# Performance work log

Hardware: AMD Instinct MI355X
Metric: run time of the kernel (lower is better)

Reference implementation:

```python
import jax, jax.numpy as jnp
import numpy as np

B, C, H, W = 8, 256, 96, 96
GH, GW = 16, 16                # proto_grid
KH, KW = H // GH, W // GW      # avg-pool kernel = stride
P = GH * GW                    # local prototypes per sample
THRESH = 0.95
NORM_EPS = 1e-4


def _safe_norm(x, axis):
    # L2-normalize with norm clamped below at NORM_EPS (matches safe_norm)
    n = jnp.sqrt(jnp.sum(x * x, axis=axis, keepdims=True))
    return x / jnp.maximum(n, NORM_EPS)


def _avg_pool(x):
    # [B, c, H, W] -> [B, c, P] non-overlapping KHxKW average pooling
    b, c = x.shape[:2]
    return x.reshape(b, c, GH, KH, GW, KW).mean(axis=(3, 5)).reshape(b, c, P)


def setup_inputs() -> dict:
    key = jax.random.key(0)
    k1, k2, k3, k4 = jax.random.split(key, 4)
    qry_fts = jax.random.normal(k1, (B, C, H, W), dtype=jnp.float32)
    sup_fts = jax.random.normal(k2, (B, C, H, W), dtype=jnp.float32)
    sup_mask = (jax.random.uniform(k3, (B, 1, H, W)) > 0.02).astype(jnp.float32)
    true_bg_mask = (jax.random.uniform(k4, (B, 1, H, W)) > 0.9).astype(jnp.float32)
    return {"qry_fts": qry_fts, "sup_fts": sup_fts,
            "sup_mask": sup_mask, "true_bg_mask": true_bg_mask}


def reference(qry_fts, sup_fts, sup_mask, true_bg_mask):
    # mode='gridconv+' path, vectorized: ragged prototype selection -> masked softmax
    local_fts = _avg_pool(sup_fts).transpose(0, 2, 1)       # [B, P, C]
    local_mask = _avg_pool(sup_mask)[:, 0, :]               # [B, P]
    local_bg = _avg_pool(true_bg_mask)[:, 0, :]             # [B, P]
    valid = (local_mask > THRESH) & (local_bg < 0.5)        # [B, P] bool

    # global masked-average prototype
    gproto = jnp.sum(sup_fts * sup_mask, axis=(-1, -2)) / (
        jnp.sum(sup_mask, axis=(-1, -2)) + 1e-5)            # [B, C]

    protos = jnp.concatenate([local_fts, gproto[:, None, :]], axis=1)  # [B, P+1, C]
    valid_all = jnp.concatenate(
        [valid, jnp.ones((B, 1), dtype=bool)], axis=1)      # global always valid

    protos_n = _safe_norm(protos, axis=2)                   # [B, P+1, C]
    qry_n = _safe_norm(qry_fts, axis=1)                     # [B, C, H, W]

    # 1x1 conv with prototype weights == batched cosine similarity
    dists = jnp.einsum('bchw,bpc->bphw', qry_n, protos_n)   # [B, P+1, H, W]

    # softmax restricted to valid prototypes (invalid get weight 0)
    logits = jnp.where(valid_all[:, :, None, None], dists, -jnp.inf)
    w = jax.nn.softmax(logits, axis=1)
    pred = jnp.sum(w * dists, axis=1, keepdims=True)        # [B, 1, H, W]
    return pred
```

## Files before the change

### kernel.cpp

```cpp
#include <hip/hip_runtime.h>

#define BB 8
#define CC 256
#define HH 96
#define WW 96
#define HWW (HH*WW)
#define NLOC 256
#define PPAD 257
#define THRESH 0.95f
#define NORM_EPS 1e-4f

typedef __attribute__((ext_vector_type(8))) _Float16 f16x8;
typedef __attribute__((ext_vector_type(16))) float f32x16;

union H16 { _Float16 f; unsigned short u; };

__global__ void k01(const float* __restrict__ sup_fts,
                    const float* __restrict__ sup_mask,
                    const float* __restrict__ true_bg,
                    float* __restrict__ protos,
                    float* __restrict__ validf,
                    float* __restrict__ masksum) {
    __shared__ float red[256];
    int blk = blockIdx.x;
    int t = threadIdx.x;
    if (blk < BB * CC) {
        int b = blk >> 8, c = blk & 255;
        int gy = t >> 4, gx = t & 15;
        const float* fb = sup_fts + ((size_t)b * CC + c) * HWW;
        const float* mb = sup_mask + (size_t)b * HWW;
        int base = gy * 6 * WW + gx * 6;
        float fs = 0.f, fm = 0.f;
        for (int r = 0; r < 6; ++r) {
            const float* rowf = fb + base + r * WW;
            const float* rowm = mb + base + r * WW;
#pragma unroll
            for (int h = 0; h < 3; ++h) {
                float2 v  = *(const float2*)(rowf + 2 * h);
                float2 mk = *(const float2*)(rowm + 2 * h);
                fs += v.x + v.y;
                fm = fmaf(v.x, mk.x, fm);
                fm = fmaf(v.y, mk.y, fm);
            }
        }
        protos[((size_t)b * PPAD + t) * CC + c] = fs * (1.f / 36.f);
        red[t] = fm;
        __syncthreads();
        for (int off = 128; off > 0; off >>= 1) {
            if (t < off) red[t] += red[t + off];
            __syncthreads();
        }
        if (t == 0) protos[((size_t)b * PPAD + 256) * CC + c] = red[0];
    } else {
        int b = blk - BB * CC;
        int gy = t >> 4, gx = t & 15;
        const float* mb = sup_mask + (size_t)b * HWW;
        const float* gb = true_bg  + (size_t)b * HWW;
        int base = gy * 6 * WW + gx * 6;
        float ms = 0.f, bs = 0.f;
        for (int r = 0; r < 6; ++r) {
            const float* rowm = mb + base + r * WW;
            const float* rowg = gb + base + r * WW;
#pragma unroll
            for (int h = 0; h < 3; ++h) {
                float2 mk = *(const float2*)(rowm + 2 * h);
                float2 bg2 = *(const float2*)(rowg + 2 * h);
                ms += mk.x + mk.y;
                bs += bg2.x + bg2.y;
            }
        }
        float mmean = ms * (1.f / 36.f);
        float bmean = bs * (1.f / 36.f);
        validf[b * PPAD + t] = (mmean > THRESH && bmean < 0.5f) ? 1.f : 0.f;
        if (t == 0) validf[b * PPAD + 256] = 1.f;
        red[t] = ms;
        __syncthreads();
        for (int off = 128; off > 0; off >>= 1) {
            if (t < off) red[t] += red[t + off];
            __syncthreads();
        }
        if (t == 0) masksum[b] = red[0];
    }
}

__global__ void k2_norm(float* __restrict__ protos,
                        const float* __restrict__ masksum,
                        unsigned short* __restrict__ Pimg) {
    int bp = blockIdx.x;
    int b = bp / PPAD;
    int p = bp - b * PPAD;
    int t = threadIdx.x;
    float v = protos[((size_t)b * PPAD + p) * CC + t];
    if (p == 256) v = v / (masksum[b] + 1e-5f);
    __shared__ float red[256];
    red[t] = v * v;
    __syncthreads();
    for (int off = 128; off > 0; off >>= 1) {
        if (t < off) red[t] += red[t + off];
        __syncthreads();
    }
    float norm = sqrtf(red[0]);
    float vn = v / fmaxf(norm, NORM_EPS);
    protos[((size_t)b * PPAD + p) * CC + t] = vn;
    if (p < NLOC) {
        H16 h; h.f = (_Float16)vn;
        int kstep = t >> 4, khalf = (t >> 3) & 1, e = t & 7;
        int tile = p >> 5, col = p & 31;
        size_t idx = ((((size_t)b * 16 + kstep) * 2 + khalf) * 8 + tile) * 256
                     + col * 8 + e;
        Pimg[idx] = h.u;
    }
}

__global__ __launch_bounds__(256, 6)
void k3_mfma(const float* __restrict__ qry,
             const unsigned short* __restrict__ Pimg,
             const float* __restrict__ protos_n,
             const float* __restrict__ validf,
             float* __restrict__ out) {
    __shared__ alignas(16) unsigned short Qf[64 * 128];
    __shared__ float red_n[8][32], red_g[8][32];
    __shared__ float rn_s[32], gd_s[32];
    __shared__ float S_l[4][32], N_l[4][32];

    int blk = blockIdx.x;
    int b = blk & 7;
    int tpx = blk >> 3;
    int px0 = tpx * 32;
    int t = threadIdx.x;
    int l = t & 63;
    int w = t >> 6;
    int col = l & 31;
    int h = l >> 5;

    int spx = t & 31;
    int cg  = t >> 5;

    const float* qb = qry + (size_t)b * CC * HWW + px0 + spx;
    const float* gp = protos_n + ((size_t)b * PPAD + 256) * CC;
    const unsigned short* Pb = Pimg + (size_t)b * 65536;

    float nrm = 0.f, gac = 0.f;
#pragma unroll
    for (int j = 0; j < 8; ++j) {
        int c0 = cg * 32 + j * 4;
        float v[4], gpv[4];
#pragma unroll
        for (int i = 0; i < 4; ++i) { v[i] = qb[(size_t)(c0 + i) * HWW]; gpv[i] = gp[c0 + i]; }
        unsigned int hh[4];
#pragma unroll
        for (int i = 0; i < 4; ++i) {
            H16 x; x.f = (_Float16)v[i];
            hh[i] = x.u;
            nrm = fmaf(v[i], v[i], nrm);
            gac = fmaf(v[i], gpv[i], gac);
        }
        int kq = cg * 8 + j;
        uint2 pk;
        pk.x = hh[0] | (hh[1] << 16); pk.y = hh[2] | (hh[3] << 16);
        *(uint2*)&Qf[kq * 128 + spx * 4] = pk;
    }
    red_n[cg][spx] = nrm;
    red_g[cg][spx] = gac;
    __syncthreads();
    if (t < 32) {
        float n2 = 0.f, gs = 0.f;
#pragma unroll
        for (int i = 0; i < 8; ++i) { n2 += red_n[i][t]; gs += red_g[i][t]; }
        float rn = 1.f / fmaxf(sqrtf(n2), NORM_EPS);
        rn_s[t] = rn;
        gd_s[t] = gs * rn;
    }

    f32x16 acc[2];
#pragma unroll
    for (int i = 0; i < 16; ++i) { acc[0][i] = 0.f; acc[1][i] = 0.f; }
    f16x8 Bf[2][2];

#define LOADB(KS, BUF)                                                        \
    {                                                                         \
        _Pragma("unroll")                                                     \
        for (int ti = 0; ti < 2; ++ti)                                        \
            Bf[BUF][ti] = *(const f16x8*)(Pb +                                \
                ((((size_t)(KS) * 2 + h) * 8 + (w * 2 + ti)) * 32 + col) * 8);\
    }

    LOADB(0, 0);
    LOADB(1, 1);

#pragma unroll
    for (int ks = 0; ks < 16; ++ks) {
        int kq0 = ks * 4 + h * 2;
        uint2 a0 = *(const uint2*)&Qf[kq0 * 128 + col * 4];
        uint2 a1 = *(const uint2*)&Qf[(kq0 + 1) * 128 + col * 4];
        union { f16x8 v; unsigned int u[4]; } QA;
        QA.u[0] = a0.x; QA.u[1] = a0.y; QA.u[2] = a1.x; QA.u[3] = a1.y;
#pragma unroll
        for (int ti = 0; ti < 2; ++ti)
            acc[ti] = __builtin_amdgcn_mfma_f32_32x32x16_f16(QA.v, Bf[ks & 1][ti], acc[ti], 0, 0, 0);
        if (ks + 2 < 16) LOADB(ks + 2, ks & 1);
    }
#undef LOADB

    __syncthreads();

    float vf0 = validf[b * PPAD + w * 64 + col];
    float vf1 = validf[b * PPAD + w * 64 + 32 + col];
#pragma unroll
    for (int r = 0; r < 16; ++r) {
        int row = (r & 3) + 8 * (r >> 2) + 4 * h;
        float rnv = rn_s[row];
        float d0 = acc[0][r] * rnv;
        float d1 = acc[1][r] * rnv;
        float l0 = (vf0 != 0.f) ? d0 : -1e30f;
        float l1 = (vf1 != 0.f) ? d1 : -1e30f;
        float e0 = __expf(l0 - 1.1f);
        float e1 = __expf(l1 - 1.1f);
        float s = e0 + e1;
        float nn = fmaf(e0, l0, e1 * l1);
#pragma unroll
        for (int m = 1; m < 32; m <<= 1) {
            s  += __shfl_xor(s, m);
            nn += __shfl_xor(nn, m);
        }
        if (col == 0) { S_l[w][row] = s; N_l[w][row] = nn; }
    }
    __syncthreads();

    if (t < 32) {
        float gdv = gd_s[t];
        float eg = __expf(gdv - 1.1f);
        float S = eg, N = eg * gdv;
#pragma unroll
        for (int i = 0; i < 4; ++i) { S += S_l[i][t]; N += N_l[i][t]; }
        out[(size_t)b * HWW + px0 + t] = N / S;
    }
}

extern "C" void kernel_launch(void* const* d_in, const int* in_sizes, int n_in,
                              void* d_out, int out_size, void* d_ws, size_t ws_size,
                              hipStream_t stream) {
    const float* qry = (const float*)d_in[0];
    const float* sup = (const float*)d_in[1];
    const float* msk = (const float*)d_in[2];
    const float* bg  = (const float*)d_in[3];
    float* out = (float*)d_out;

    float* ws = (float*)d_ws;
    float* protos  = ws;
    float* validf  = protos + (size_t)BB * PPAD * CC;
    float* masksum = validf + (size_t)BB * PPAD;
    unsigned short* Pimg = (unsigned short*)(masksum + BB);

    hipLaunchKernelGGL(k01, dim3(BB * CC + BB), dim3(256), 0, stream,
                       sup, msk, bg, protos, validf, masksum);
    hipLaunchKernelGGL(k2_norm, dim3(BB * PPAD), dim3(256), 0, stream, protos, masksum, Pimg);
    hipLaunchKernelGGL(k3_mfma, dim3(BB * (HWW / 32)), dim3(256), 0, stream,
                       qry, Pimg, protos, validf, out);
}
```

Baseline: 58.22 us.

## Software-pipeline query loads across three pixel tiles per block with double-buffered LDS

```diff
diff --git a/kernel.cpp b/kernel.cpp
--- a/kernel.cpp
+++ b/kernel.cpp
@@ -112,128 +112,167 @@
     }
 }
 
-__global__ __launch_bounds__(256, 6)
+#define LBAR()  do {                                             \
+        asm volatile("s_waitcnt lgkmcnt(0)" ::: "memory");       \
+        __builtin_amdgcn_sched_barrier(0);                       \
+        __builtin_amdgcn_s_barrier();                            \
+        __builtin_amdgcn_sched_barrier(0);                       \
+    } while (0)
+
+__global__ __launch_bounds__(256, 4)
 void k3_mfma(const float* __restrict__ qry,
              const unsigned short* __restrict__ Pimg,
              const float* __restrict__ protos_n,
              const float* __restrict__ validf,
              float* __restrict__ out) {
-    __shared__ alignas(16) unsigned short Qf[64 * 128];
-    __shared__ float red_n[8][32], red_g[8][32];
-    __shared__ float rn_s[32], gd_s[32];
+    __shared__ alignas(16) unsigned short Qf[2][8192];
+    __shared__ float red_n[2][8][32], red_g[2][8][32];
+    __shared__ float rn_s[2][32], gd_s[2][32];
     __shared__ float S_l[4][32], N_l[4][32];
 
     int blk = blockIdx.x;
     int b = blk & 7;
-    int tpx = blk >> 3;
-    int px0 = tpx * 32;
+    int tgrp = blk >> 3;
+    int pxbase = tgrp * 96;
     int t = threadIdx.x;
     int l = t & 63;
     int w = t >> 6;
     int col = l & 31;
     int h = l >> 5;
-
     int spx = t & 31;
     int cg  = t >> 5;
 
-    const float* qb = qry + (size_t)b * CC * HWW + px0 + spx;
+    const float* qB = qry + (size_t)b * CC * HWW + spx;
     const float* gp = protos_n + ((size_t)b * PPAD + 256) * CC;
     const unsigned short* Pb = Pimg + (size_t)b * 65536;
-
-    float nrm = 0.f, gac = 0.f;
-#pragma unroll
-    for (int j = 0; j < 8; ++j) {
-        int c0 = cg * 32 + j * 4;
-        float v[4], gpv[4];
-#pragma unroll
-        for (int i = 0; i < 4; ++i) { v[i] = qb[(size_t)(c0 + i) * HWW]; gpv[i] = gp[c0 + i]; }
-        unsigned int hh[4];
-#pragma unroll
-        for (int i = 0; i < 4; ++i) {
-            H16 x; x.f = (_Float16)v[i];
-            hh[i] = x.u;
-            nrm = fmaf(v[i], v[i], nrm);
-            gac = fmaf(v[i], gpv[i], gac);
-        }
-        int kq = cg * 8 + j;
-        uint2 pk;
-        pk.x = hh[0] | (hh[1] << 16); pk.y = hh[2] | (hh[3] << 16);
-        *(uint2*)&Qf[kq * 128 + spx * 4] = pk;
-    }
-    red_n[cg][spx] = nrm;
-    red_g[cg][spx] = gac;
-    __syncthreads();
-    if (t < 32) {
-        float n2 = 0.f, gs = 0.f;
-#pragma unroll
-        for (int i = 0; i < 8; ++i) { n2 += red_n[i][t]; gs += red_g[i][t]; }
-        float rn = 1.f / fmaxf(sqrtf(n2), NORM_EPS);
-        rn_s[t] = rn;
-        gd_s[t] = gs * rn;
-    }
-
-    f32x16 acc[2];
-#pragma unroll
-    for (int i = 0; i < 16; ++i) { acc[0][i] = 0.f; acc[1][i] = 0.f; }
-    f16x8 Bf[2][2];
-
-#define LOADB(KS, BUF)                                                        \
-    {                                                                         \
+    float* outb = out + (size_t)b * HWW + pxbase;
+
+    float vfl0 = validf[b * PPAD + w * 64 + col];
+    float vfl1 = validf[b * PPAD + w * 64 + 32 + col];
+
+    {
+        float nrm = 0.f, gac = 0.f;
+        const float* qb = qB + pxbase;
+#pragma unroll
+        for (int j = 0; j < 8; ++j) {
+            int c0 = cg * 32 + j * 4;
+            float v[4];
+#pragma unroll
+            for (int i = 0; i < 4; ++i) v[i] = qb[(size_t)(c0 + i) * HWW];
+            unsigned int hh[4];
+#pragma unroll
+            for (int i = 0; i < 4; ++i) {
+                H16 x; x.f = (_Float16)v[i];
+                hh[i] = x.u;
+                nrm = fmaf(v[i], v[i], nrm);
+                gac = fmaf(v[i], gp[c0 + i], gac);
+            }
+            uint2 pk;
+            pk.x = hh[0] | (hh[1] << 16); pk.y = hh[2] | (hh[3] << 16);
+            *(uint2*)&Qf[0][(cg * 8 + j) * 128 + spx * 4] = pk;
+        }
+        red_n[0][cg][spx] = nrm;
+        red_g[0][cg][spx] = gac;
+    }
+
+#pragma unroll
+    for (int ti = 0; ti < 3; ++ti) {
+        const int p = ti & 1;
+        LBAR();
+        if (t < 32) {
+            float n2 = 0.f, gs = 0.f;
+#pragma unroll
+            for (int i = 0; i < 8; ++i) { n2 += red_n[p][i][t]; gs += red_g[p][i][t]; }
+            float rn = 1.f / fmaxf(sqrtf(n2), NORM_EPS);
+            rn_s[p][t] = rn;
+            gd_s[p][t] = gs * rn;
+        }
+        LBAR();
+
+        f32x16 acc[2];
+#pragma unroll
+        for (int i = 0; i < 16; ++i) { acc[0][i] = 0.f; acc[1][i] = 0.f; }
+        f16x8 Bf[2][2];
+        float qv[4][4], gpv[4][4];
+        float nrm = 0.f, gac = 0.f;
+        const float* qbn = qB + pxbase + (ti + 1) * 32;
+
+#define LOADB(KS, BUF) { _Pragma("unroll")                                    \
+        for (int tix = 0; tix < 2; ++tix)                                     \
+            Bf[BUF][tix] = *(const f16x8*)(Pb +                               \
+                ((((size_t)(KS) * 2 + h) * 8 + (w * 2 + tix)) * 32 + col) * 8); }
+
+#define QISSUE(J) { int c0 = cg * 32 + (J) * 4;                               \
         _Pragma("unroll")                                                     \
-        for (int ti = 0; ti < 2; ++ti)                                        \
-            Bf[BUF][ti] = *(const f16x8*)(Pb +                                \
-                ((((size_t)(KS) * 2 + h) * 8 + (w * 2 + ti)) * 32 + col) * 8);\
-    }
-
-    LOADB(0, 0);
-    LOADB(1, 1);
-
-#pragma unroll
-    for (int ks = 0; ks < 16; ++ks) {
-        int kq0 = ks * 4 + h * 2;
-        uint2 a0 = *(const uint2*)&Qf[kq0 * 128 + col * 4];
-        uint2 a1 = *(const uint2*)&Qf[(kq0 + 1) * 128 + col * 4];
-        union { f16x8 v; unsigned int u[4]; } QA;
-        QA.u[0] = a0.x; QA.u[1] = a0.y; QA.u[2] = a1.x; QA.u[3] = a1.y;
-#pragma unroll
-        for (int ti = 0; ti < 2; ++ti)
-            acc[ti] = __builtin_amdgcn_mfma_f32_32x32x16_f16(QA.v, Bf[ks & 1][ti], acc[ti], 0, 0, 0);
-        if (ks + 2 < 16) LOADB(ks + 2, ks & 1);
-    }
+        for (int i = 0; i < 4; ++i) {                                         \
+            qv[(J) & 3][i]  = qbn[(size_t)(c0 + i) * HWW];                    \
+            gpv[(J) & 3][i] = gp[c0 + i]; } }
+
+#define QCONV(J) { unsigned int hh[4];                                        \
+        _Pragma("unroll")                                                     \
+        for (int i = 0; i < 4; ++i) {                                         \
+            float v = qv[(J) & 3][i];                                         \
+            H16 x; x.f = (_Float16)v; hh[i] = x.u;                            \
+            nrm = fmaf(v, v, nrm);                                            \
+            gac = fmaf(v, gpv[(J) & 3][i], gac); }                            \
+        uint2 pk; pk.x = hh[0] | (hh[1] << 16); pk.y = hh[2] | (hh[3] << 16); \
+        *(uint2*)&Qf[1 - p][(cg * 8 + (J)) * 128 + spx * 4] = pk; }
+
+        LOADB(0, 0);
+        LOADB(1, 1);
+#pragma unroll
+        for (int ks = 0; ks < 16; ++ks) {
+            int kq0 = ks * 4 + h * 2;
+            uint2 a0 = *(const uint2*)&Qf[p][kq0 * 128 + col * 4];
+            uint2 a1 = *(const uint2*)&Qf[p][(kq0 + 1) * 128 + col * 4];
+            union { f16x8 v; unsigned int u[4]; } QA;
+            QA.u[0] = a0.x; QA.u[1] = a0.y; QA.u[2] = a1.x; QA.u[3] = a1.y;
+#pragma unroll
+            for (int tix = 0; tix < 2; ++tix)
+                acc[tix] = __builtin_amdgcn_mfma_f32_32x32x16_f16(QA.v, Bf[ks & 1][tix], acc[tix], 0, 0, 0);
+            if (ks + 2 < 16) LOADB(ks + 2, ks & 1);
+            if (ti < 2 && (ks & 1) == 0) {
+                if (ks >= 8) QCONV((ks >> 1) - 4);
+                QISSUE(ks >> 1);
+            }
+        }
+        if (ti < 2) {
+            QCONV(4); QCONV(5); QCONV(6); QCONV(7);
+            red_n[1 - p][cg][spx] = nrm;
+            red_g[1 - p][cg][spx] = gac;
+        }
 #undef LOADB
-
-    __syncthreads();
-
-    float vf0 = validf[b * PPAD + w * 64 + col];
-    float vf1 = validf[b * PPAD + w * 64 + 32 + col];
-#pragma unroll
-    for (int r = 0; r < 16; ++r) {
-        int row = (r & 3) + 8 * (r >> 2) + 4 * h;
-        float rnv = rn_s[row];
-        float d0 = acc[0][r] * rnv;
-        float d1 = acc[1][r] * rnv;
-        float l0 = (vf0 != 0.f) ? d0 : -1e30f;
-        float l1 = (vf1 != 0.f) ? d1 : -1e30f;
-        float e0 = __expf(l0 - 1.1f);
-        float e1 = __expf(l1 - 1.1f);
-        float s = e0 + e1;
-        float nn = fmaf(e0, l0, e1 * l1);
-#pragma unroll
-        for (int m = 1; m < 32; m <<= 1) {
-            s  += __shfl_xor(s, m);
-            nn += __shfl_xor(nn, m);
-        }
-        if (col == 0) { S_l[w][row] = s; N_l[w][row] = nn; }
-    }
-    __syncthreads();
-
-    if (t < 32) {
-        float gdv = gd_s[t];
-        float eg = __expf(gdv - 1.1f);
-        float S = eg, N = eg * gdv;
-#pragma unroll
-        for (int i = 0; i < 4; ++i) { S += S_l[i][t]; N += N_l[i][t]; }
-        out[(size_t)b * HWW + px0 + t] = N / S;
+#undef QISSUE
+#undef QCONV
+
+#pragma unroll
+        for (int r = 0; r < 16; ++r) {
+            int row = (r & 3) + 8 * (r >> 2) + 4 * h;
+            float rnv = rn_s[p][row];
+            float d0 = acc[0][r] * rnv;
+            float d1 = acc[1][r] * rnv;
+            float l0 = (vfl0 != 0.f) ? d0 : -1e30f;
+            float l1 = (vfl1 != 0.f) ? d1 : -1e30f;
+            float e0 = __expf(l0 - 1.1f);
+            float e1 = __expf(l1 - 1.1f);
+            float s = e0 + e1;
+            float nn = fmaf(e0, l0, e1 * l1);
+#pragma unroll
+            for (int m = 1; m < 32; m <<= 1) {
+                s  += __shfl_xor(s, m);
+                nn += __shfl_xor(nn, m);
+            }
+            if (col == 0) { S_l[w][row] = s; N_l[w][row] = nn; }
+        }
+        LBAR();
+        if (t < 32) {
+            float gdv = gd_s[p][t];
+            float eg = __expf(gdv - 1.1f);
+            float S = eg, N = eg * gdv;
+#pragma unroll
+            for (int i = 0; i < 4; ++i) { S += S_l[i][t]; N += N_l[i][t]; }
+            outb[ti * 32 + t] = N / S;
+        }
     }
 }
 
@@ -255,6 +294,6 @@
     hipLaunchKernelGGL(k01, dim3(BB * CC + BB), dim3(256), 0, stream,
                        sup, msk, bg, protos, validf, masksum);
     hipLaunchKernelGGL(k2_norm, dim3(BB * PPAD), dim3(256), 0, stream, protos, masksum, Pimg);
-    hipLaunchKernelGGL(k3_mfma, dim3(BB * (HWW / 32)), dim3(256), 0, stream,
+    hipLaunchKernelGGL(k3_mfma, dim3(BB * 96), dim3(256), 0, stream,
                        qry, Pimg, protos, validf, out);
 }
```

Result: slower. 79.79 us (+37.0%).

## Split query fp16 conversion into separate pre-pass kernel with tiled image

Applied to the files above, without the earlier changes.

```diff
diff --git a/kernel.cpp b/kernel.cpp
--- a/kernel.cpp
+++ b/kernel.cpp
@@ -112,97 +112,132 @@
     }
 }
 
-__global__ __launch_bounds__(256, 6)
-void k3_mfma(const float* __restrict__ qry,
+__global__ __launch_bounds__(256, 4)
+void k2q(const float* __restrict__ qry,
+         const float* __restrict__ protos_n,
+         unsigned short* __restrict__ Qimg,
+         float* __restrict__ rns,
+         float* __restrict__ gds) {
+    __shared__ alignas(16) unsigned short T[64 * 64 * 4];
+    __shared__ float gpl[256];
+    __shared__ float rn4[4][64], rg4[4][64];
+
+    int blk = blockIdx.x;
+    int b = blk / 144;
+    int tp = blk - b * 144;
+    int px0 = tp * 64;
+    int t = threadIdx.x;
+    int px = t & 63;
+    int cq = t >> 6;
+
+    const float* gp = protos_n + ((size_t)b * PPAD + 256) * CC;
+    gpl[t] = gp[t];
+    __syncthreads();
+
+    const float* qb = qry + (size_t)b * CC * HWW + px0 + px;
+    float nrm = 0.f, gac = 0.f;
+#pragma unroll
+    for (int j = 0; j < 16; ++j) {
+        int c0 = cq * 64 + j * 4;
+        unsigned int hh[4];
+#pragma unroll
+        for (int i = 0; i < 4; ++i) {
+            float v = qb[(size_t)(c0 + i) * HWW];
+            H16 x; x.f = (_Float16)v;
+            hh[i] = x.u;
+            nrm = fmaf(v, v, nrm);
+            gac = fmaf(v, gpl[c0 + i], gac);
+        }
+        uint2 pk;
+        pk.x = hh[0] | (hh[1] << 16); pk.y = hh[2] | (hh[3] << 16);
+        int kq = cq * 16 + j;
+        *(uint2*)&T[(kq * 64 + px) * 4] = pk;
+    }
+    rn4[cq][px] = nrm;
+    rg4[cq][px] = gac;
+    __syncthreads();
+    if (t < 64) {
+        float n2 = rn4[0][t] + rn4[1][t] + rn4[2][t] + rn4[3][t];
+        float gs = rg4[0][t] + rg4[1][t] + rg4[2][t] + rg4[3][t];
+        float rn = 1.f / fmaxf(sqrtf(n2), NORM_EPS);
+        rns[(size_t)b * HWW + px0 + t] = rn;
+        gds[(size_t)b * HWW + px0 + t] = gs * rn;
+    }
+
+    unsigned short* Qo = Qimg + ((size_t)b * 288 + (size_t)tp * 2) * 8192;
+#pragma unroll
+    for (int r = 0; r < 16; ++r) {
+        int F = r * 256 + t;
+        int kq = F >> 6, pxx = F & 63;
+        uint2 v = *(const uint2*)&T[(kq * 64 + pxx) * 4];
+        int tile = pxx >> 5, pl = pxx & 31;
+        *(uint2*)&Qo[(size_t)tile * 8192 + (kq * 32 + pl) * 4] = v;
+    }
+}
+
+__global__ __launch_bounds__(256, 4)
+void k3_mfma(const unsigned short* __restrict__ Qimg,
              const unsigned short* __restrict__ Pimg,
-             const float* __restrict__ protos_n,
+             const float* __restrict__ rns,
+             const float* __restrict__ gds,
              const float* __restrict__ validf,
              float* __restrict__ out) {
-    __shared__ alignas(16) unsigned short Qf[64 * 128];
-    __shared__ float red_n[8][32], red_g[8][32];
+    __shared__ alignas(16) unsigned short Qf[8192];
     __shared__ float rn_s[32], gd_s[32];
     __shared__ float S_l[4][32], N_l[4][32];
 
     int blk = blockIdx.x;
     int b = blk & 7;
-    int tpx = blk >> 3;
-    int px0 = tpx * 32;
+    int tile = blk >> 3;
+    int px0 = tile * 32;
     int t = threadIdx.x;
     int l = t & 63;
     int w = t >> 6;
     int col = l & 31;
     int h = l >> 5;
 
-    int spx = t & 31;
-    int cg  = t >> 5;
-
-    const float* qb = qry + (size_t)b * CC * HWW + px0 + spx;
-    const float* gp = protos_n + ((size_t)b * PPAD + 256) * CC;
+    const unsigned short* Qt = Qimg + ((size_t)b * 288 + tile) * 8192;
     const unsigned short* Pb = Pimg + (size_t)b * 65536;
 
-    float nrm = 0.f, gac = 0.f;
-#pragma unroll
-    for (int j = 0; j < 8; ++j) {
-        int c0 = cg * 32 + j * 4;
-        float v[4], gpv[4];
-#pragma unroll
-        for (int i = 0; i < 4; ++i) { v[i] = qb[(size_t)(c0 + i) * HWW]; gpv[i] = gp[c0 + i]; }
-        unsigned int hh[4];
-#pragma unroll
-        for (int i = 0; i < 4; ++i) {
-            H16 x; x.f = (_Float16)v[i];
-            hh[i] = x.u;
-            nrm = fmaf(v[i], v[i], nrm);
-            gac = fmaf(v[i], gpv[i], gac);
-        }
-        int kq = cg * 8 + j;
-        uint2 pk;
-        pk.x = hh[0] | (hh[1] << 16); pk.y = hh[2] | (hh[3] << 16);
-        *(uint2*)&Qf[kq * 128 + spx * 4] = pk;
-    }
-    red_n[cg][spx] = nrm;
-    red_g[cg][spx] = gac;
-    __syncthreads();
+    {
+        const char* src = (const char*)Qt + t * 16;
+        char* dst = (char*)Qf + (t >> 6) * 1024;
+#pragma unroll
+        for (int i = 0; i < 4; ++i)
+            __builtin_amdgcn_global_load_lds((const void*)(src + i * 4096),
+                                             (void*)(dst + i * 4096), 16, 0, 0);
+    }
     if (t < 32) {
-        float n2 = 0.f, gs = 0.f;
-#pragma unroll
-        for (int i = 0; i < 8; ++i) { n2 += red_n[i][t]; gs += red_g[i][t]; }
-        float rn = 1.f / fmaxf(sqrtf(n2), NORM_EPS);
-        rn_s[t] = rn;
-        gd_s[t] = gs * rn;
-    }
+        rn_s[t] = rns[(size_t)b * HWW + px0 + t];
+        gd_s[t] = gds[(size_t)b * HWW + px0 + t];
+    }
+    __syncthreads();
 
     f32x16 acc[2];
 #pragma unroll
     for (int i = 0; i < 16; ++i) { acc[0][i] = 0.f; acc[1][i] = 0.f; }
-    f16x8 Bf[2][2];
-
-#define LOADB(KS, BUF)                                                        \
-    {                                                                         \
-        _Pragma("unroll")                                                     \
-        for (int ti = 0; ti < 2; ++ti)                                        \
-            Bf[BUF][ti] = *(const f16x8*)(Pb +                                \
-                ((((size_t)(KS) * 2 + h) * 8 + (w * 2 + ti)) * 32 + col) * 8);\
-    }
-
-    LOADB(0, 0);
-    LOADB(1, 1);
+    f16x8 Bf[4][2];
+
+#define LOADB(KS, BUF) { _Pragma("unroll")                                    \
+        for (int tix = 0; tix < 2; ++tix)                                     \
+            Bf[BUF][tix] = *(const f16x8*)(Pb +                               \
+                ((((size_t)(KS) * 2 + h) * 8 + (w * 2 + tix)) * 32 + col) * 8); }
+
+    LOADB(0, 0); LOADB(1, 1); LOADB(2, 2); LOADB(3, 3);
 
 #pragma unroll
     for (int ks = 0; ks < 16; ++ks) {
         int kq0 = ks * 4 + h * 2;
-        uint2 a0 = *(const uint2*)&Qf[kq0 * 128 + col * 4];
-        uint2 a1 = *(const uint2*)&Qf[(kq0 + 1) * 128 + col * 4];
+        uint2 a0 = *(const uint2*)&Qf[(kq0 * 32 + col) * 4];
+        uint2 a1 = *(const uint2*)&Qf[((kq0 + 1) * 32 + col) * 4];
         union { f16x8 v; unsigned int u[4]; } QA;
         QA.u[0] = a0.x; QA.u[1] = a0.y; QA.u[2] = a1.x; QA.u[3] = a1.y;
 #pragma unroll
-        for (int ti = 0; ti < 2; ++ti)
-            acc[ti] = __builtin_amdgcn_mfma_f32_32x32x16_f16(QA.v, Bf[ks & 1][ti], acc[ti], 0, 0, 0);
-        if (ks + 2 < 16) LOADB(ks + 2, ks & 1);
+        for (int tix = 0; tix < 2; ++tix)
+            acc[tix] = __builtin_amdgcn_mfma_f32_32x32x16_f16(QA.v, Bf[ks & 3][tix], acc[tix], 0, 0, 0);
+        if (ks + 4 < 16) LOADB(ks + 4, ks & 3);
     }
 #undef LOADB
-
-    __syncthreads();
 
     float vf0 = validf[b * PPAD + w * 64 + col];
     float vf1 = validf[b * PPAD + w * 64 + 32 + col];
@@ -250,11 +285,16 @@
     float* protos  = ws;
     float* validf  = protos + (size_t)BB * PPAD * CC;
     float* masksum = validf + (size_t)BB * PPAD;
-    unsigned short* Pimg = (unsigned short*)(masksum + BB);
+    float* rns     = masksum + BB;
+    float* gds     = rns + (size_t)BB * HWW;
+    unsigned short* Pimg = (unsigned short*)(gds + (size_t)BB * HWW);
+    unsigned short* Qimg = Pimg + (size_t)BB * 65536;
 
     hipLaunchKernelGGL(k01, dim3(BB * CC + BB), dim3(256), 0, stream,
                        sup, msk, bg, protos, validf, masksum);
     hipLaunchKernelGGL(k2_norm, dim3(BB * PPAD), dim3(256), 0, stream, protos, masksum, Pimg);
+    hipLaunchKernelGGL(k2q, dim3(BB * 144), dim3(256), 0, stream,
+                       qry, protos, Qimg, rns, gds);
     hipLaunchKernelGGL(k3_mfma, dim3(BB * (HWW / 32)), dim3(256), 0, stream,
-                       qry, Pimg, protos, validf, out);
-}
+                       Qimg, Pimg, rns, gds, validf, out);
+}
```

Result: slower. 74.31 us (+27.6%).

## Process 64 pixels per block in similarity kernel to reuse prototype fragments

Applied to the files above, without the earlier changes.

```diff
diff --git a/kernel.cpp b/kernel.cpp
--- a/kernel.cpp
+++ b/kernel.cpp
@@ -112,69 +112,75 @@
     }
 }
 
-__global__ __launch_bounds__(256, 6)
+__global__ __launch_bounds__(256, 4)
 void k3_mfma(const float* __restrict__ qry,
              const unsigned short* __restrict__ Pimg,
              const float* __restrict__ protos_n,
              const float* __restrict__ validf,
              float* __restrict__ out) {
-    __shared__ alignas(16) unsigned short Qf[64 * 128];
-    __shared__ float red_n[8][32], red_g[8][32];
-    __shared__ float rn_s[32], gd_s[32];
-    __shared__ float S_l[4][32], N_l[4][32];
+    __shared__ alignas(16) unsigned short Qf[64 * 256];
+    __shared__ float red_n[4][64], red_g[4][64];
+    __shared__ float rn_s[64], gd_s[64];
+    __shared__ float S_l[4][64], N_l[4][64];
 
     int blk = blockIdx.x;
     int b = blk & 7;
-    int tpx = blk >> 3;
-    int px0 = tpx * 32;
+    int tile = blk >> 3;
+    int px0 = tile * 64;
     int t = threadIdx.x;
     int l = t & 63;
     int w = t >> 6;
     int col = l & 31;
     int h = l >> 5;
 
-    int spx = t & 31;
-    int cg  = t >> 5;
+    int spx = t & 63;
+    int cq  = t >> 6;
 
     const float* qb = qry + (size_t)b * CC * HWW + px0 + spx;
     const float* gp = protos_n + ((size_t)b * PPAD + 256) * CC;
     const unsigned short* Pb = Pimg + (size_t)b * 65536;
 
+    float vf0 = validf[b * PPAD + w * 64 + col];
+    float vf1 = validf[b * PPAD + w * 64 + 32 + col];
+
     float nrm = 0.f, gac = 0.f;
 #pragma unroll
-    for (int j = 0; j < 8; ++j) {
-        int c0 = cg * 32 + j * 4;
-        float v[4], gpv[4];
-#pragma unroll
-        for (int i = 0; i < 4; ++i) { v[i] = qb[(size_t)(c0 + i) * HWW]; gpv[i] = gp[c0 + i]; }
-        unsigned int hh[4];
-#pragma unroll
-        for (int i = 0; i < 4; ++i) {
+    for (int g8 = 0; g8 < 8; ++g8) {
+        int c0 = cq * 64 + g8 * 8;
+        float v[8];
+#pragma unroll
+        for (int i = 0; i < 8; ++i) v[i] = qb[(size_t)(c0 + i) * HWW];
+        unsigned int hh[8];
+#pragma unroll
+        for (int i = 0; i < 8; ++i) {
             H16 x; x.f = (_Float16)v[i];
             hh[i] = x.u;
             nrm = fmaf(v[i], v[i], nrm);
-            gac = fmaf(v[i], gpv[i], gac);
-        }
-        int kq = cg * 8 + j;
-        uint2 pk;
-        pk.x = hh[0] | (hh[1] << 16); pk.y = hh[2] | (hh[3] << 16);
-        *(uint2*)&Qf[kq * 128 + spx * 4] = pk;
-    }
-    red_n[cg][spx] = nrm;
-    red_g[cg][spx] = gac;
-    __syncthreads();
-    if (t < 32) {
-        float n2 = 0.f, gs = 0.f;
-#pragma unroll
-        for (int i = 0; i < 8; ++i) { n2 += red_n[i][t]; gs += red_g[i][t]; }
+            gac = fmaf(v[i], gp[c0 + i], gac);
+        }
+        int kq = cq * 16 + g8 * 2;
+        uint2 p0, p1;
+        p0.x = hh[0] | (hh[1] << 16); p0.y = hh[2] | (hh[3] << 16);
+        p1.x = hh[4] | (hh[5] << 16); p1.y = hh[6] | (hh[7] << 16);
+        *(uint2*)&Qf[kq * 256 + spx * 4] = p0;
+        *(uint2*)&Qf[(kq + 1) * 256 + spx * 4] = p1;
+    }
+    red_n[cq][spx] = nrm;
+    red_g[cq][spx] = gac;
+    __syncthreads();
+    if (t < 64) {
+        float n2 = red_n[0][t] + red_n[1][t] + red_n[2][t] + red_n[3][t];
+        float gs = red_g[0][t] + red_g[1][t] + red_g[2][t] + red_g[3][t];
         float rn = 1.f / fmaxf(sqrtf(n2), NORM_EPS);
         rn_s[t] = rn;
         gd_s[t] = gs * rn;
     }
 
-    f32x16 acc[2];
-#pragma unroll
-    for (int i = 0; i < 16; ++i) { acc[0][i] = 0.f; acc[1][i] = 0.f; }
+    f32x16 acc[2][2];
+#pragma unroll
+    for (int s = 0; s < 2; ++s)
+#pragma unroll
+        for (int i = 0; i < 16; ++i) { acc[s][0][i] = 0.f; acc[s][1][i] = 0.f; }
     f16x8 Bf[2][2];
 
 #define LOADB(KS, BUF)                                                        \
@@ -191,43 +197,49 @@
 #pragma unroll
     for (int ks = 0; ks < 16; ++ks) {
         int kq0 = ks * 4 + h * 2;
-        uint2 a0 = *(const uint2*)&Qf[kq0 * 128 + col * 4];
-        uint2 a1 = *(const uint2*)&Qf[(kq0 + 1) * 128 + col * 4];
-        union { f16x8 v; unsigned int u[4]; } QA;
-        QA.u[0] = a0.x; QA.u[1] = a0.y; QA.u[2] = a1.x; QA.u[3] = a1.y;
-#pragma unroll
-        for (int ti = 0; ti < 2; ++ti)
-            acc[ti] = __builtin_amdgcn_mfma_f32_32x32x16_f16(QA.v, Bf[ks & 1][ti], acc[ti], 0, 0, 0);
+        uint2 a0 = *(const uint2*)&Qf[kq0 * 256 + col * 4];
+        uint2 a1 = *(const uint2*)&Qf[(kq0 + 1) * 256 + col * 4];
+        uint2 a2 = *(const uint2*)&Qf[kq0 * 256 + (32 + col) * 4];
+        uint2 a3 = *(const uint2*)&Qf[(kq0 + 1) * 256 + (32 + col) * 4];
+        union { f16x8 v; unsigned int u[4]; } Q0, Q1;
+        Q0.u[0] = a0.x; Q0.u[1] = a0.y; Q0.u[2] = a1.x; Q0.u[3] = a1.y;
+        Q1.u[0] = a2.x; Q1.u[1] = a2.y; Q1.u[2] = a3.x; Q1.u[3] = a3.y;
+#pragma unroll
+        for (int ti = 0; ti < 2; ++ti) {
+            acc[0][ti] = __builtin_amdgcn_mfma_f32_32x32x16_f16(Q0.v, Bf[ks & 1][ti], acc[0][ti], 0, 0, 0);
+            acc[1][ti] = __builtin_amdgcn_mfma_f32_32x32x16_f16(Q1.v, Bf[ks & 1][ti], acc[1][ti], 0, 0, 0);
+        }
         if (ks + 2 < 16) LOADB(ks + 2, ks & 1);
     }
 #undef LOADB
 
     __syncthreads();
 
-    float vf0 = validf[b * PPAD + w * 64 + col];
-    float vf1 = validf[b * PPAD + w * 64 + 32 + col];
-#pragma unroll
-    for (int r = 0; r < 16; ++r) {
-        int row = (r & 3) + 8 * (r >> 2) + 4 * h;
-        float rnv = rn_s[row];
-        float d0 = acc[0][r] * rnv;
-        float d1 = acc[1][r] * rnv;
-        float l0 = (vf0 != 0.f) ? d0 : -1e30f;
-        float l1 = (vf1 != 0.f) ? d1 : -1e30f;
-        float e0 = __expf(l0 - 1.1f);
-        float e1 = __expf(l1 - 1.1f);
-        float s = e0 + e1;
-        float nn = fmaf(e0, l0, e1 * l1);
-#pragma unroll
-        for (int m = 1; m < 32; m <<= 1) {
-            s  += __shfl_xor(s, m);
-            nn += __shfl_xor(nn, m);
-        }
-        if (col == 0) { S_l[w][row] = s; N_l[w][row] = nn; }
-    }
-    __syncthreads();
-
-    if (t < 32) {
+#pragma unroll
+    for (int sub = 0; sub < 2; ++sub) {
+#pragma unroll
+        for (int r = 0; r < 16; ++r) {
+            int row = sub * 32 + (r & 3) + 8 * (r >> 2) + 4 * h;
+            float rnv = rn_s[row];
+            float d0 = acc[sub][0][r] * rnv;
+            float d1 = acc[sub][1][r] * rnv;
+            float l0 = (vf0 != 0.f) ? d0 : -1e30f;
+            float l1 = (vf1 != 0.f) ? d1 : -1e30f;
+            float e0 = __expf(l0 - 1.1f);
+            float e1 = __expf(l1 - 1.1f);
+            float s = e0 + e1;
+            float nn = fmaf(e0, l0, e1 * l1);
+#pragma unroll
+            for (int m = 1; m < 32; m <<= 1) {
+                s  += __shfl_xor(s, m);
+                nn += __shfl_xor(nn, m);
+            }
+            if (col == 0) { S_l[w][row] = s; N_l[w][row] = nn; }
+        }
+    }
+    __syncthreads();
+
+    if (t < 64) {
         float gdv = gd_s[t];
         float eg = __expf(gdv - 1.1f);
         float S = eg, N = eg * gdv;
@@ -255,6 +267,6 @@
     hipLaunchKernelGGL(k01, dim3(BB * CC + BB), dim3(256), 0, stream,
                        sup, msk, bg, protos, validf, masksum);
     hipLaunchKernelGGL(k2_norm, dim3(BB * PPAD), dim3(256), 0, stream, protos, masksum, Pimg);
-    hipLaunchKernelGGL(k3_mfma, dim3(BB * (HWW / 32)), dim3(256), 0, stream,
+    hipLaunchKernelGGL(k3_mfma, dim3(BB * (HWW / 64)), dim3(256), 0, stream,
                        qry, Pimg, protos, validf, out);
 }
```

Measured after the change: 67.84 us. +16.5%, slower.
